# Kernel tuning notes

Measured on AMD Instinct MI355X. Metric: run time of the kernel, lower is better.

Reference implementation:

```python
import jax, jax.numpy as jnp
import numpy as np

B, CIN, COUT, RES, WDIM, K = 16, 512, 512, 64, 512, 3
LRELU_ALPHA = 0.2
ACT_GAIN = float(np.sqrt(2.0))  # bias_act def_gain for lrelu


def setup_inputs() -> dict:
    key = jax.random.key(0)
    ks = jax.random.split(key, 8)
    return {
        "x": jax.random.normal(ks[0], (B, CIN, RES, RES), dtype=jnp.float32),
        "w": jax.random.normal(ks[1], (B, WDIM), dtype=jnp.float32),
        "weight": jax.random.normal(ks[2], (COUT, CIN, K, K), dtype=jnp.float32),
        "bias": jnp.zeros((COUT,), dtype=jnp.float32),
        "affine_w": jax.random.normal(ks[3], (CIN, WDIM), dtype=jnp.float32),
        "affine_b": jnp.ones((CIN,), dtype=jnp.float32),  # bias_init=1
        "noise_const": jax.random.normal(ks[4], (RES, RES), dtype=jnp.float32),
        "noise_strength": jnp.asarray(0.1, dtype=jnp.float32),
    }


def reference(x, w, weight, bias, affine_w, affine_b, noise_const, noise_strength):
    # affine: FullyConnectedLayer with lr-equalized weight scale 1/sqrt(w_dim)
    styles = w @ (affine_w.T * (1.0 / np.sqrt(WDIM))) + affine_b  # [B, CIN]

    # modulate: per-sample scaled weights [B, COUT, CIN, K, K]
    wmod = weight[None] * styles[:, None, :, None, None]
    # demodulate
    demod = jax.lax.rsqrt(jnp.sum(wmod * wmod, axis=(2, 3, 4)) + 1e-8)  # [B, COUT]
    wmod = wmod * demod[:, :, None, None, None]

    # per-sample conv2d, padding=k//2 (StyleGAN2 groups=batch trick -> vmap)
    def conv1(xi, wi):
        return jax.lax.conv_general_dilated(
            xi[None], wi, window_strides=(1, 1),
            padding=[(K // 2, K // 2), (K // 2, K // 2)],
            dimension_numbers=("NCHW", "OIHW", "NCHW"))[0]

    y = jax.vmap(conv1)(x, wmod)  # [B, COUT, RES, RES]

    # noise injection (noise_mode='const'): broadcast [RES,RES] over batch/channel
    y = y + noise_const * noise_strength

    # fused bias + lrelu + gain (conv_clamp=None)
    y = y + bias[None, :, None, None]
    y = jnp.where(y >= 0, y, LRELU_ALPHA * y) * ACT_GAIN
    return y
```

## Files before the change

kernel.cpp:

```cpp
#include <hip/hip_runtime.h>
#include <hip/hip_bf16.h>

#define B_     16
#define CIN_   512
#define COUT_  512
#define RES_   64
#define WDIM_  512
#define LRELU_A 0.2f
#define GAIN_  1.4142135623730951f

typedef __attribute__((ext_vector_type(8)))  __bf16 bf16x8;
typedef __attribute__((ext_vector_type(16))) float  f32x16;
typedef __attribute__((ext_vector_type(4)))  int    int4v;
typedef __attribute__((ext_vector_type(8)))  unsigned short u16x8;

__device__ __forceinline__ unsigned short f2bf(float f) {
    union { float f; unsigned int u; } v; v.f = f;
    unsigned int u = v.u;
    return (unsigned short)((u + 0x7FFFu + ((u >> 16) & 1u)) >> 16);
}

__device__ __forceinline__ void gl_lds16(const void* g, void* l) {
    __builtin_amdgcn_global_load_lds(
        (const __attribute__((address_space(1))) unsigned int*)g,
        (__attribute__((address_space(3))) unsigned int*)l, 16, 0, 0);
}

__global__ void zero_k(unsigned short* __restrict__ xs) {
    int idx = blockIdx.x * 256 + threadIdx.x;
    int b = idx >> 13, side = (idx >> 12) & 1, off = idx & 4095;
    int4v z = {0, 0, 0, 0};
    *(int4v*)((char*)xs + ((size_t)(b * 66 + side * 65) * 4096 + off) * 16) = z;
}

__global__ void styles_k(const float* __restrict__ w, const float* __restrict__ aw,
                         const float* __restrict__ ab, float* __restrict__ styles) {
    int idx = blockIdx.x * 256 + threadIdx.x;
    int b = idx >> 9, ci = idx & 511;
    const float4* wp = (const float4*)(w + b * WDIM_);
    const float4* ap = (const float4*)(aw + (size_t)ci * WDIM_);
    float acc = 0.f;
    #pragma unroll 4
    for (int k = 0; k < WDIM_ / 4; ++k) {
        float4 a = ap[k], q = wp[k];
        acc += a.x * q.x + a.y * q.y + a.z * q.z + a.w * q.w;
    }
    styles[idx] = acc * 0.04419417382415922f + ab[ci];
}

__global__ void wprep_k(const float* __restrict__ weight, unsigned short* __restrict__ wt,
                        float* __restrict__ wsq) {
    int idx = blockIdx.x * 256 + threadIdx.x;
    int co = idx >> 9, ci = idx & 511;
    const float* wp = weight + (size_t)idx * 9;
    float s = 0.f;
    #pragma unroll
    for (int t = 0; t < 9; ++t) {
        float f = wp[t];
        s += f * f;
        wt[(((size_t)(ci >> 4) * 9 + t) * 512 + co) * 16 + (ci & 15)] = f2bf(f);
    }
    wsq[idx] = s;
}

__global__ void demod_k(const float* __restrict__ styles, const float* __restrict__ wsq,
                        float* __restrict__ demod) {
    int idx = blockIdx.x * 256 + threadIdx.x;
    int b = idx >> 9, co = idx & 511;
    const float4* wr = (const float4*)(wsq + (size_t)co * CIN_);
    const float4* sr = (const float4*)(styles + (size_t)b * CIN_);
    float acc = 0.f;
    #pragma unroll 4
    for (int ci = 0; ci < CIN_ / 4; ++ci) {
        float4 q = wr[ci], s = sr[ci];
        acc += q.x * s.x * s.x + q.y * s.y * s.y + q.z * s.z * s.z + q.w * s.w * s.w;
    }
    demod[idx] = rsqrtf(acc + 1e-8f);
}

__global__ void xprep_k(const float* __restrict__ x, const float* __restrict__ styles,
                        unsigned short* __restrict__ xs) {
    __shared__ float tile[64][65];
    __shared__ float styv[64];
    int bid = blockIdx.x;
    int ct = bid & 7, h = (bid >> 3) & 63, b = bid >> 9;
    int tid = threadIdx.x;
    if (tid < 64) styv[tid] = styles[b * CIN_ + ct * 64 + tid];
    const float* xp = x + (((size_t)(b * CIN_ + ct * 64)) * RES_ + h) * RES_;
    #pragma unroll
    for (int it = 0; it < 4; ++it) {
        int ci = it * 16 + (tid >> 4);
        int w4 = (tid & 15) * 4;
        float4 v = *(const float4*)(xp + (size_t)ci * (RES_ * RES_) + w4);
        tile[ci][w4] = v.x; tile[ci][w4 + 1] = v.y; tile[ci][w4 + 2] = v.z; tile[ci][w4 + 3] = v.w;
    }
    __syncthreads();
    unsigned short* xo = xs + (size_t)(b * 66 + h + 1) * 32768 + (size_t)ct * 4096;
    #pragma unroll
    for (int it = 0; it < 2; ++it) {
        int s = it * 256 + tid;
        int ccl = s >> 7, w = (s >> 1) & 63, half = s & 1;
        int ci0 = ccl * 16 + half * 8;
        u16x8 v;
        #pragma unroll
        for (int j = 0; j < 8; ++j) v[j] = f2bf(tile[ci0 + j][w] * styv[ci0 + j]);
        *(u16x8*)(xo + ccl * 1024 + w * 16 + half * 8) = v;
    }
}

#define WBUF 36864
#define XBUF 12672
#define LDS_TOTAL (WBUF + 2*XBUF)

__global__ __launch_bounds__(256, 2) void conv_k(
    const unsigned short* __restrict__ xs, const unsigned short* __restrict__ wt,
    const float* __restrict__ demod, const float* __restrict__ bias,
    const float* __restrict__ noise, const float* __restrict__ nsp,
    float* __restrict__ out)
{
    extern __shared__ char lds[];
    char* Wl = lds;
    char* Xl = lds + WBUF;

    const int tid  = threadIdx.x;
    const int lane = tid & 63;
    const int wid  = tid >> 6;
    const int l31  = lane & 31;
    const int kg   = lane >> 5;

    const int lb = ((blockIdx.x & 7) << 7) | (blockIdx.x >> 3);
    const int m  = lb >> 8;
    const int rest = lb & 255;
    const int b  = rest >> 4;
    const int h0 = (rest & 15) * 4;

    if (tid < 48) {
        int buf = tid / 24, rem = tid % 24, r = rem >> 2, k = rem & 3;
        int chunk = r * 132 + (k < 2 ? k : 128 + k);
        int4v z = {0, 0, 0, 0};
        *(int4v*)(Xl + buf * XBUF + chunk * 16) = z;
    }

    const char* wsrc = (const char*)wt + (size_t)m * (128 * 32);
    auto stageW = [&](int cc) {
        const char* s0 = wsrc + (size_t)cc * (9 * 512 * 32);
        #pragma unroll
        for (int k = 0; k < 9; ++k) {
            const int c0 = k * 256 + (wid << 6);
            const int c  = c0 + lane;
            const int sc = c ^ ((c >> 3) & 1);
            gl_lds16(s0 + (size_t)(sc >> 8) * 16384 + (size_t)(sc & 255) * 16,
                     Wl + c0 * 16);
        }
    };
    const char* xsrc = (const char*)xs + (size_t)(b * 66 + h0) * 65536;
    auto stageX = [&](int cc, int buf) {
        const char* s0 = xsrc + cc * 2048;
        char* d0 = Xl + buf * XBUF;
        #pragma unroll
        for (int k = 0; k < 3; ++k) {
            const int c0 = k * 256 + (wid << 6);
            const int r  = c0 >> 7;
            const int cw = ((c0 + lane) & 127) + 2;
            const int sw = cw ^ ((cw >> 3) & 1);
            gl_lds16(s0 + (size_t)r * 65536 + (size_t)(sw - 2) * 16,
                     d0 + (r * 132 + ((c0 & 127) + 2)) * 16);
        }
    };

    f32x16 acc[4][2];
    #pragma unroll
    for (int mt = 0; mt < 4; ++mt)
        #pragma unroll
        for (int nt = 0; nt < 2; ++nt)
            #pragma unroll
            for (int j = 0; j < 16; ++j) acc[mt][nt][j] = 0.f;

    stageW(0);
    stageX(0, 0);
    asm volatile("s_waitcnt vmcnt(0)" ::: "memory");
    __syncthreads();

    int xb = 0;
    for (int cc = 0; cc < 32; ++cc) {
        if (cc < 31) stageX(cc + 1, xb ^ 1);
        const char* Xb = Xl + xb * XBUF;
        #pragma unroll
        for (int t = 0; t < 9; ++t) {
            const int dy = t / 3, dx = t % 3;
            bf16x8 af[4], bv[2];
            #pragma unroll
            for (int mt = 0; mt < 4; ++mt) {
                int o = (mt * 32 + l31) * 32 + (kg << 4);
                o ^= (o >> 3) & 16;
                af[mt] = *(const bf16x8*)(Wl + t * 4096 + o);
            }
            #pragma unroll
            for (int nt = 0; nt < 2; ++nt) {
                int site = nt * 32 + l31 + dx;
                int o = site * 32 + (kg << 4);
                o ^= (o >> 3) & 16;
                bv[nt] = *(const bf16x8*)(Xb + (wid + dy) * 2112 + o);
            }
            #pragma unroll
            for (int mt = 0; mt < 4; ++mt)
                #pragma unroll
                for (int nt = 0; nt < 2; ++nt)
                    acc[mt][nt] = __builtin_amdgcn_mfma_f32_32x32x16_bf16(
                        af[mt], bv[nt], acc[mt][nt], 0, 0, 0);
        }
        if (cc < 31) {
            __builtin_amdgcn_sched_barrier(0);
            __builtin_amdgcn_s_barrier();
            stageW(cc + 1);
            asm volatile("s_waitcnt vmcnt(0)" ::: "memory");
            __builtin_amdgcn_s_barrier();
            __builtin_amdgcn_sched_barrier(0);
        }
        xb ^= 1;
    }

    const float nsv = nsp[0];
    const int h = h0 + wid;
    const float* dm = demod + b * COUT_ + m * 128;
    float nz[2];
    nz[0] = noise[h * 64 + l31] * nsv;
    nz[1] = noise[h * 64 + 32 + l31] * nsv;
    #pragma unroll
    for (int mt = 0; mt < 4; ++mt) {
        #pragma unroll
        for (int j = 0; j < 16; ++j) {
            int row = (j & 3) + 8 * (j >> 2) + 4 * kg;
            int co  = mt * 32 + row;
            float d  = dm[co];
            float bs = bias[m * 128 + co];
            #pragma unroll
            for (int nt = 0; nt < 2; ++nt) {
                float v = acc[mt][nt][j] * d + nz[nt] + bs;
                v = (v >= 0.f ? v : LRELU_A * v) * GAIN_;
                out[((size_t)(b * COUT_ + m * 128 + co) * RES_ + h) * RES_ + nt * 32 + l31] = v;
            }
        }
    }
}

extern "C" void kernel_launch(void* const* d_in, const int* in_sizes, int n_in,
                              void* d_out, int out_size, void* d_ws, size_t ws_size,
                              hipStream_t stream) {
    const float* x    = (const float*)d_in[0];
    const float* w    = (const float*)d_in[1];
    const float* wgt  = (const float*)d_in[2];
    const float* bias = (const float*)d_in[3];
    const float* aw   = (const float*)d_in[4];
    const float* ab   = (const float*)d_in[5];
    const float* noi  = (const float*)d_in[6];
    const float* ns   = (const float*)d_in[7];
    float* out = (float*)d_out;

    char* ws = (char*)d_ws;
    float* styles        = (float*)(ws);
    float* demod         = (float*)(ws + 32768);
    float* wsq           = (float*)(ws + 65536);
    unsigned short* wt   = (unsigned short*)(ws + 1114112);
    unsigned short* xs   = (unsigned short*)(ws + 6291456);

    hipLaunchKernelGGL(zero_k,   dim3(512),  dim3(256), 0, stream, xs);
    hipLaunchKernelGGL(styles_k, dim3(32),   dim3(256), 0, stream, w, aw, ab, styles);
    hipLaunchKernelGGL(wprep_k,  dim3(1024), dim3(256), 0, stream, wgt, wt, wsq);
    hipLaunchKernelGGL(xprep_k,  dim3(8192), dim3(256), 0, stream, x, styles, xs);
    hipLaunchKernelGGL(demod_k,  dim3(32),   dim3(256), 0, stream, styles, wsq, demod);

    hipFuncSetAttribute((const void*)conv_k, hipFuncAttributeMaxDynamicSharedMemorySize, LDS_TOTAL);
    hipLaunchKernelGGL(conv_k, dim3(1024), dim3(256), LDS_TOTAL, stream,
                       xs, wt, demod, bias, noi, ns, out);
}
```

Measured before the change: 528.4 us.

## Pipeline weight staging in double-buffered thirds overlapped with MFMA compute

Weight tiles for each input-channel chunk are now staged one third (one kernel row) at a time into a two-slot ring, instead of all nine taps at once into a single buffer. Each step reads its fragments from LDS into registers first, then issues async global-to-LDS loads for the next third and the next X tile. It then runs the MFMAs at raised wave priority and waits only for the weight loads before the barrier. The aim is to hide the weight-load latency and the stall-heavy barrier of the old layout behind matrix work, and to shrink the weight LDS footprint. The cost is more barriers per chunk and higher register pressure from holding three taps of fragments. The prologue also drops its explicit vmcnt wait before the first barrier, which could race.

```diff
diff --git a/kernel.cpp b/kernel.cpp
--- a/kernel.cpp
+++ b/kernel.cpp
@@ -108,9 +108,9 @@
     }
 }
 
-#define WBUF 36864
-#define XBUF 12672
-#define LDS_TOTAL (WBUF + 2*XBUF)
+#define WTHIRD 12288
+#define XBUF   12672
+#define LDS_TOTAL (2*WTHIRD + 2*XBUF)
 
 __global__ __launch_bounds__(256, 2) void conv_k(
     const unsigned short* __restrict__ xs, const unsigned short* __restrict__ wt,
@@ -120,7 +120,7 @@
 {
     extern __shared__ char lds[];
     char* Wl = lds;
-    char* Xl = lds + WBUF;
+    char* Xl = lds + 2 * WTHIRD;
 
     const int tid  = threadIdx.x;
     const int lane = tid & 63;
@@ -142,15 +142,16 @@
     }
 
     const char* wsrc = (const char*)wt + (size_t)m * (128 * 32);
-    auto stageW = [&](int cc) {
-        const char* s0 = wsrc + (size_t)cc * (9 * 512 * 32);
-        #pragma unroll
-        for (int k = 0; k < 9; ++k) {
+    auto stageW3 = [&](int cc2, int t2, int dh) {
+        const char* s0 = wsrc + (size_t)cc2 * 147456 + (size_t)t2 * 49152;
+        char* d0 = Wl + dh * WTHIRD;
+        #pragma unroll
+        for (int k = 0; k < 3; ++k) {
             const int c0 = k * 256 + (wid << 6);
             const int c  = c0 + lane;
             const int sc = c ^ ((c >> 3) & 1);
             gl_lds16(s0 + (size_t)(sc >> 8) * 16384 + (size_t)(sc & 255) * 16,
-                     Wl + c0 * 16);
+                     d0 + c0 * 16);
         }
     };
     const char* xsrc = (const char*)xs + (size_t)(b * 66 + h0) * 65536;
@@ -176,48 +177,62 @@
             #pragma unroll
             for (int j = 0; j < 16; ++j) acc[mt][nt][j] = 0.f;
 
-    stageW(0);
+    stageW3(0, 0, 0);
     stageX(0, 0);
-    asm volatile("s_waitcnt vmcnt(0)" ::: "memory");
     __syncthreads();
 
-    int xb = 0;
     for (int cc = 0; cc < 32; ++cc) {
-        if (cc < 31) stageX(cc + 1, xb ^ 1);
+        const int xb = cc & 1;
         const char* Xb = Xl + xb * XBUF;
         #pragma unroll
-        for (int t = 0; t < 9; ++t) {
-            const int dy = t / 3, dx = t % 3;
-            bf16x8 af[4], bv[2];
-            #pragma unroll
-            for (int mt = 0; mt < 4; ++mt) {
-                int o = (mt * 32 + l31) * 32 + (kg << 4);
-                o ^= (o >> 3) & 16;
-                af[mt] = *(const bf16x8*)(Wl + t * 4096 + o);
-            }
-            #pragma unroll
-            for (int nt = 0; nt < 2; ++nt) {
-                int site = nt * 32 + l31 + dx;
-                int o = site * 32 + (kg << 4);
-                o ^= (o >> 3) & 16;
-                bv[nt] = *(const bf16x8*)(Xb + (wid + dy) * 2112 + o);
-            }
-            #pragma unroll
-            for (int mt = 0; mt < 4; ++mt)
+        for (int t = 0; t < 3; ++t) {
+            const int wh = (cc + t) & 1;
+            const char* Wb = Wl + wh * WTHIRD;
+
+            bf16x8 af[3][4], bv[3][2];
+            #pragma unroll
+            for (int tt = 0; tt < 3; ++tt) {
                 #pragma unroll
-                for (int nt = 0; nt < 2; ++nt)
-                    acc[mt][nt] = __builtin_amdgcn_mfma_f32_32x32x16_bf16(
-                        af[mt], bv[nt], acc[mt][nt], 0, 0, 0);
-        }
-        if (cc < 31) {
-            __builtin_amdgcn_sched_barrier(0);
-            __builtin_amdgcn_s_barrier();
-            stageW(cc + 1);
-            asm volatile("s_waitcnt vmcnt(0)" ::: "memory");
-            __builtin_amdgcn_s_barrier();
-            __builtin_amdgcn_sched_barrier(0);
-        }
-        xb ^= 1;
+                for (int mt = 0; mt < 4; ++mt) {
+                    int o = (tt * 128 + mt * 32 + l31) * 32 + (kg << 4);
+                    o ^= (o >> 3) & 16;
+                    af[tt][mt] = *(const bf16x8*)(Wb + o);
+                }
+                #pragma unroll
+                for (int nt = 0; nt < 2; ++nt) {
+                    int o = (nt * 32 + l31 + tt) * 32 + (kg << 4);
+                    o ^= (o >> 3) & 16;
+                    bv[tt][nt] = *(const bf16x8*)(Xb + (wid + t) * 2112 + o);
+                }
+            }
+
+            const int p = cc * 3 + t;
+            const bool stX = (t == 0) && (cc < 31);
+            if (p < 95) {
+                const int cc2 = (t == 2) ? cc + 1 : cc;
+                const int t2  = (t == 2) ? 0 : t + 1;
+                stageW3(cc2, t2, wh ^ 1);
+            }
+            if (stX) stageX(cc + 1, xb ^ 1);
+
+            __builtin_amdgcn_s_setprio(1);
+            #pragma unroll
+            for (int tt = 0; tt < 3; ++tt)
+                #pragma unroll
+                for (int mt = 0; mt < 4; ++mt)
+                    #pragma unroll
+                    for (int nt = 0; nt < 2; ++nt)
+                        acc[mt][nt] = __builtin_amdgcn_mfma_f32_32x32x16_bf16(
+                            af[tt][mt], bv[tt][nt], acc[mt][nt], 0, 0, 0);
+            __builtin_amdgcn_s_setprio(0);
+
+            if (p < 95) {
+                if (stX) asm volatile("s_waitcnt vmcnt(3)" ::: "memory");
+                else     asm volatile("s_waitcnt vmcnt(0)" ::: "memory");
+                __builtin_amdgcn_s_barrier();
+                __builtin_amdgcn_sched_barrier(0);
+            }
+        }
     }
 
     const float nsv = nsp[0];
```

New measurement: 540.7 us. +2.3%, slower.

## Load conv weights straight to registers and retile waves for wider N

Applied to the files above, without the earlier changes.

The conv kernel no longer stages modulated weights through LDS. Each wave now loads its A fragments directly from global memory into double-buffered registers one phase ahead, and X keeps its LDS double buffer with fewer barriers. Waves are retiled to cover 64 output channels by 2 rows × 64 columns (2x4 MFMA tiles), MFMA sections get raised priority, and the XOR swizzle on X is dropped. Padding-row zeroing is folded into xprep, which removes one launch. This targets LDS traffic and barrier stalls from weight staging, at the cost of more registers and global/L2 weight loads per wave, and possible LDS bank conflicts now that X is unswizzled.

```diff
diff --git a/kernel.cpp b/kernel.cpp
--- a/kernel.cpp
+++ b/kernel.cpp
@@ -24,13 +24,6 @@
     __builtin_amdgcn_global_load_lds(
         (const __attribute__((address_space(1))) unsigned int*)g,
         (__attribute__((address_space(3))) unsigned int*)l, 16, 0, 0);
-}
-
-__global__ void zero_k(unsigned short* __restrict__ xs) {
-    int idx = blockIdx.x * 256 + threadIdx.x;
-    int b = idx >> 13, side = (idx >> 12) & 1, off = idx & 4095;
-    int4v z = {0, 0, 0, 0};
-    *(int4v*)((char*)xs + ((size_t)(b * 66 + side * 65) * 4096 + off) * 16) = z;
 }
 
 __global__ void styles_k(const float* __restrict__ w, const float* __restrict__ aw,
@@ -83,8 +76,20 @@
     __shared__ float tile[64][65];
     __shared__ float styv[64];
     int bid = blockIdx.x;
-    int ct = bid & 7, h = (bid >> 3) & 63, b = bid >> 9;
+    int ct = bid & 7, rr = (bid >> 3) % 66, b = bid / 528;
     int tid = threadIdx.x;
+    unsigned short* xo = xs + (size_t)(b * 66 + rr) * 32768 + (size_t)ct * 4096;
+    if (rr == 0 || rr == 65) {
+        u16x8 z = {0, 0, 0, 0, 0, 0, 0, 0};
+        #pragma unroll
+        for (int it = 0; it < 2; ++it) {
+            int s = it * 256 + tid;
+            int ccl = s >> 7, w = (s >> 1) & 63, half = s & 1;
+            *(u16x8*)(xo + ccl * 1024 + w * 16 + half * 8) = z;
+        }
+        return;
+    }
+    int h = rr - 1;
     if (tid < 64) styv[tid] = styles[b * CIN_ + ct * 64 + tid];
     const float* xp = x + (((size_t)(b * CIN_ + ct * 64)) * RES_ + h) * RES_;
     #pragma unroll
@@ -95,7 +100,6 @@
         tile[ci][w4] = v.x; tile[ci][w4 + 1] = v.y; tile[ci][w4 + 2] = v.z; tile[ci][w4 + 3] = v.w;
     }
     __syncthreads();
-    unsigned short* xo = xs + (size_t)(b * 66 + h + 1) * 32768 + (size_t)ct * 4096;
     #pragma unroll
     for (int it = 0; it < 2; ++it) {
         int s = it * 256 + tid;
@@ -108,9 +112,32 @@
     }
 }
 
-#define WBUF 36864
 #define XBUF 12672
-#define LDS_TOTAL (WBUF + 2*XBUF)
+
+#define LOADAF(PH, CC, DY) do {                                              \
+    const char* p_ = wb_ + (size_t)((CC) * 9 + (DY) * 3) * 16384;            \
+    _Pragma("unroll") for (int tt_ = 0; tt_ < 3; ++tt_)                      \
+      _Pragma("unroll") for (int mt_ = 0; mt_ < 2; ++mt_)                    \
+        af[PH][tt_][mt_] = *(const bf16x8*)(p_ + tt_ * 16384 + mt_ * 1024);  \
+  } while (0)
+
+#define PHASE(CC, DY, PH, NPH, NCC, NDY, GUARD) do {                         \
+    const char* Xb = Xl + ((CC) & 1) * XBUF;                                 \
+    bf16x8 bv[3][4];                                                         \
+    _Pragma("unroll") for (int tt_ = 0; tt_ < 3; ++tt_)                      \
+      _Pragma("unroll") for (int nt_ = 0; nt_ < 4; ++nt_) {                  \
+        int o_ = (((nt_ & 1) * 32) + l31 + tt_) * 32 + (kg << 4);            \
+        bv[tt_][nt_] = *(const bf16x8*)(Xb + (rp * 2 + (nt_ >> 1) + (DY)) * 2112 + o_); \
+      }                                                                      \
+    if (GUARD) { LOADAF(NPH, NCC, NDY); }                                    \
+    __builtin_amdgcn_s_setprio(1);                                           \
+    _Pragma("unroll") for (int tt_ = 0; tt_ < 3; ++tt_)                      \
+      _Pragma("unroll") for (int mt_ = 0; mt_ < 2; ++mt_)                    \
+        _Pragma("unroll") for (int nt_ = 0; nt_ < 4; ++nt_)                  \
+          acc[mt_][nt_] = __builtin_amdgcn_mfma_f32_32x32x16_bf16(           \
+              af[PH][tt_][mt_], bv[tt_][nt_], acc[mt_][nt_], 0, 0, 0);       \
+    __builtin_amdgcn_s_setprio(0);                                           \
+  } while (0)
 
 __global__ __launch_bounds__(256, 2) void conv_k(
     const unsigned short* __restrict__ xs, const unsigned short* __restrict__ wt,
@@ -118,15 +145,15 @@
     const float* __restrict__ noise, const float* __restrict__ nsp,
     float* __restrict__ out)
 {
-    extern __shared__ char lds[];
-    char* Wl = lds;
-    char* Xl = lds + WBUF;
+    __shared__ __align__(16) char Xl[2 * XBUF];
 
     const int tid  = threadIdx.x;
     const int lane = tid & 63;
     const int wid  = tid >> 6;
     const int l31  = lane & 31;
     const int kg   = lane >> 5;
+    const int ch   = wid & 1;
+    const int rp   = wid >> 1;
 
     const int lb = ((blockIdx.x & 7) << 7) | (blockIdx.x >> 3);
     const int m  = lb >> 8;
@@ -141,18 +168,6 @@
         *(int4v*)(Xl + buf * XBUF + chunk * 16) = z;
     }
 
-    const char* wsrc = (const char*)wt + (size_t)m * (128 * 32);
-    auto stageW = [&](int cc) {
-        const char* s0 = wsrc + (size_t)cc * (9 * 512 * 32);
-        #pragma unroll
-        for (int k = 0; k < 9; ++k) {
-            const int c0 = k * 256 + (wid << 6);
-            const int c  = c0 + lane;
-            const int sc = c ^ ((c >> 3) & 1);
-            gl_lds16(s0 + (size_t)(sc >> 8) * 16384 + (size_t)(sc & 255) * 16,
-                     Wl + c0 * 16);
-        }
-    };
     const char* xsrc = (const char*)xs + (size_t)(b * 66 + h0) * 65536;
     auto stageX = [&](int cc, int buf) {
         const char* s0 = xsrc + cc * 2048;
@@ -161,84 +176,61 @@
         for (int k = 0; k < 3; ++k) {
             const int c0 = k * 256 + (wid << 6);
             const int r  = c0 >> 7;
-            const int cw = ((c0 + lane) & 127) + 2;
-            const int sw = cw ^ ((cw >> 3) & 1);
-            gl_lds16(s0 + (size_t)r * 65536 + (size_t)(sw - 2) * 16,
+            gl_lds16(s0 + (size_t)r * 65536 + (size_t)((c0 + lane) & 127) * 16,
                      d0 + (r * 132 + ((c0 & 127) + 2)) * 16);
         }
     };
 
-    f32x16 acc[4][2];
-    #pragma unroll
-    for (int mt = 0; mt < 4; ++mt)
-        #pragma unroll
-        for (int nt = 0; nt < 2; ++nt)
+    const char* wb_ = (const char*)wt
+        + (size_t)((m * 128 + ch * 64 + l31) * 32 + kg * 16);
+
+    f32x16 acc[2][4];
+    #pragma unroll
+    for (int mt = 0; mt < 2; ++mt)
+        #pragma unroll
+        for (int nt = 0; nt < 4; ++nt)
             #pragma unroll
             for (int j = 0; j < 16; ++j) acc[mt][nt][j] = 0.f;
 
-    stageW(0);
+    bf16x8 af[2][3][2];
+
     stageX(0, 0);
-    asm volatile("s_waitcnt vmcnt(0)" ::: "memory");
+    LOADAF(0, 0, 0);
     __syncthreads();
 
-    int xb = 0;
-    for (int cc = 0; cc < 32; ++cc) {
-        if (cc < 31) stageX(cc + 1, xb ^ 1);
-        const char* Xb = Xl + xb * XBUF;
-        #pragma unroll
-        for (int t = 0; t < 9; ++t) {
-            const int dy = t / 3, dx = t % 3;
-            bf16x8 af[4], bv[2];
+    for (int pb = 0; pb < 16; ++pb) {
+        const int ccE = pb * 2, ccO = ccE + 1;
+        stageX(ccO, 1);
+        PHASE(ccE, 0, 0, 1, ccE, 1, true);
+        PHASE(ccE, 1, 1, 0, ccE, 2, true);
+        PHASE(ccE, 2, 0, 1, ccO, 0, true);
+        __syncthreads();
+        if (pb < 15) stageX(ccO + 1, 0);
+        PHASE(ccO, 0, 1, 0, ccO, 1, true);
+        PHASE(ccO, 1, 0, 1, ccO, 2, true);
+        PHASE(ccO, 2, 1, 0, ccO + 1, 0, (pb < 15));
+        if (pb < 15) __syncthreads();
+    }
+
+    const float nsv = nsp[0];
+    float nz[4];
+    #pragma unroll
+    for (int nt = 0; nt < 4; ++nt)
+        nz[nt] = noise[(h0 + rp * 2 + (nt >> 1)) * 64 + (nt & 1) * 32 + l31] * nsv;
+    #pragma unroll
+    for (int mt = 0; mt < 2; ++mt) {
+        #pragma unroll
+        for (int j = 0; j < 16; ++j) {
+            int co = m * 128 + ch * 64 + mt * 32 + (j & 3) + 8 * (j >> 2) + 4 * kg;
+            float d  = demod[b * COUT_ + co];
+            float bs = bias[co];
             #pragma unroll
-            for (int mt = 0; mt < 4; ++mt) {
-                int o = (mt * 32 + l31) * 32 + (kg << 4);
-                o ^= (o >> 3) & 16;
-                af[mt] = *(const bf16x8*)(Wl + t * 4096 + o);
-            }
-            #pragma unroll
-            for (int nt = 0; nt < 2; ++nt) {
-                int site = nt * 32 + l31 + dx;
-                int o = site * 32 + (kg << 4);
-                o ^= (o >> 3) & 16;
-                bv[nt] = *(const bf16x8*)(Xb + (wid + dy) * 2112 + o);
-            }
-            #pragma unroll
-            for (int mt = 0; mt < 4; ++mt)
-                #pragma unroll
-                for (int nt = 0; nt < 2; ++nt)
-                    acc[mt][nt] = __builtin_amdgcn_mfma_f32_32x32x16_bf16(
-                        af[mt], bv[nt], acc[mt][nt], 0, 0, 0);
-        }
-        if (cc < 31) {
-            __builtin_amdgcn_sched_barrier(0);
-            __builtin_amdgcn_s_barrier();
-            stageW(cc + 1);
-            asm volatile("s_waitcnt vmcnt(0)" ::: "memory");
-            __builtin_amdgcn_s_barrier();
-            __builtin_amdgcn_sched_barrier(0);
-        }
-        xb ^= 1;
-    }
-
-    const float nsv = nsp[0];
-    const int h = h0 + wid;
-    const float* dm = demod + b * COUT_ + m * 128;
-    float nz[2];
-    nz[0] = noise[h * 64 + l31] * nsv;
-    nz[1] = noise[h * 64 + 32 + l31] * nsv;
-    #pragma unroll
-    for (int mt = 0; mt < 4; ++mt) {
-        #pragma unroll
-        for (int j = 0; j < 16; ++j) {
-            int row = (j & 3) + 8 * (j >> 2) + 4 * kg;
-            int co  = mt * 32 + row;
-            float d  = dm[co];
-            float bs = bias[m * 128 + co];
-            #pragma unroll
-            for (int nt = 0; nt < 2; ++nt) {
+            for (int nt = 0; nt < 4; ++nt) {
+                int h = h0 + rp * 2 + (nt >> 1);
+                int w = (nt & 1) * 32 + l31;
                 float v = acc[mt][nt][j] * d + nz[nt] + bs;
                 v = (v >= 0.f ? v : LRELU_A * v) * GAIN_;
-                out[((size_t)(b * COUT_ + m * 128 + co) * RES_ + h) * RES_ + nt * 32 + l31] = v;
+                out[((size_t)(b * COUT_ + co) * RES_ + h) * RES_ + w] = v;
             }
         }
     }
@@ -264,13 +256,10 @@
     unsigned short* wt   = (unsigned short*)(ws + 1114112);
     unsigned short* xs   = (unsigned short*)(ws + 6291456);
 
-    hipLaunchKernelGGL(zero_k,   dim3(512),  dim3(256), 0, stream, xs);
     hipLaunchKernelGGL(styles_k, dim3(32),   dim3(256), 0, stream, w, aw, ab, styles);
+    hipLaunchKernelGGL(xprep_k,  dim3(8448), dim3(256), 0, stream, x, styles, xs);
     hipLaunchKernelGGL(wprep_k,  dim3(1024), dim3(256), 0, stream, wgt, wt, wsq);
-    hipLaunchKernelGGL(xprep_k,  dim3(8192), dim3(256), 0, stream, x, styles, xs);
     hipLaunchKernelGGL(demod_k,  dim3(32),   dim3(256), 0, stream, styles, wsq, demod);
-
-    hipFuncSetAttribute((const void*)conv_k, hipFuncAttributeMaxDynamicSharedMemorySize, LDS_TOTAL);
-    hipLaunchKernelGGL(conv_k, dim3(1024), dim3(256), LDS_TOTAL, stream,
+    hipLaunchKernelGGL(conv_k,   dim3(1024), dim3(256), 0, stream,
                        xs, wt, demod, bias, noi, ns, out);
 }
```

Result: no change. 536.5 us (+1.5%).
